# Kernel optimization log

Hardware: AMD Instinct MI355X
Metric: run time of the kernel (lower is better)

## Reference

```python
import jax, jax.numpy as jnp
import numpy as np

B, T, F, U = 32, 128, 128, 128  # batch, seq_length, feature dim, lstm units


def setup_inputs() -> dict:
    key = jax.random.key(0)
    ks = jax.random.split(key, 5)
    X = jax.random.normal(ks[0], (B, T, F), dtype=jnp.float32)
    # Dense(seq_length) over concat([X, s_repeated]) -> weight [(F+U), T]
    Wd = jax.random.normal(ks[1], (F + U, T), dtype=jnp.float32) / np.sqrt(F + U)
    bd = jnp.zeros((T,), jnp.float32)
    # Keras LSTM params, gate order i,f,c,o packed along last axis
    Wk = jax.random.normal(ks[2], (F, 4 * U), dtype=jnp.float32) / np.sqrt(F)
    Wr = jax.random.normal(ks[3], (U, 4 * U), dtype=jnp.float32) / np.sqrt(U)
    bl = jnp.zeros((4 * U,), jnp.float32)
    return {"X": X, "Wd": Wd, "bd": bd, "Wk": Wk, "Wr": Wr, "bl": bl}


def reference(X, Wd, bd, Wk, Wr, bl):
    Bq, Tq, Fq = X.shape
    Uq = Wr.shape[0]

    def step(s, i):
        # s: attention query carried across steps (= previous h_state)
        s_rep = jnp.broadcast_to(s[:, None, :], (Bq, Tq, Uq))
        concat_X = jnp.concatenate([X, s_rep], axis=-1)           # [B,T,F+U]
        alphas = jax.nn.softmax(concat_X @ Wd + bd, axis=1)        # [B,T,T], softmax over seq axis
        alpha_i = alphas[:, :, i]                                  # [B,T] (only column i is used)
        ctx = jnp.einsum('bt,btf->bf', alpha_i, X)                 # [B,F] weighted sum
        # Keras LSTM called with initial_state=None each step -> h0 = c0 = 0
        h0 = jnp.zeros((Bq, Uq), X.dtype)
        c0 = jnp.zeros((Bq, Uq), X.dtype)
        z = ctx @ Wk + h0 @ Wr + bl                                # [B,4U]
        zi, zf, zc, zo = jnp.split(z, 4, axis=-1)
        c = jax.nn.sigmoid(zf) * c0 + jax.nn.sigmoid(zi) * jnp.tanh(zc)
        h = jax.nn.sigmoid(zo) * jnp.tanh(c)                       # [B,U]
        return h, h  # new query s = h_state; per-step output = lstm_out[:, 0, :]

    s0 = jnp.zeros((Bq, Uq), X.dtype)
    _, outs = jax.lax.scan(step, s0, jnp.arange(Tq))               # [T,B,U]
    return jnp.transpose(outs, (1, 0, 2))                          # [B,T,U]
```

## Files before the change

### kernel.cpp

```cpp
#include <hip/hip_runtime.h>

namespace {

constexpr int Bq = 32;
constexpr int Tq = 128;
constexpr int Fq = 128;
constexpr int Uq = 128;
constexpr int PITCH = 129;
constexpr int APITCH = 17;

__device__ __forceinline__ float sigmoid_(float x) {
  return 1.0f / (1.0f + __expf(-x));
}
__device__ __forceinline__ float tanh_(float x) {
  x = fminf(20.0f, fmaxf(-20.0f, x));
  const float e = __expf(2.0f * x);
  return (e - 1.0f) / (e + 1.0f);
}

__global__ __launch_bounds__(256) void k_fused(const float* __restrict__ X,
                                               const float* __restrict__ Wd,
                                               float* __restrict__ C) {
  __shared__ float Xs[Tq * PITCH];
  __shared__ float As[Tq * APITCH];
  const int tid = threadIdx.x;
  const int b = blockIdx.y;
  const float* Xb = X + b * (Tq * Fq);
#pragma unroll
  for (int it = 0; it < 16; ++it) {
    const int e = tid + it * 256;
    const int t = e >> 5;
    const int f4 = e & 31;
    const float4 v = reinterpret_cast<const float4*>(Xb)[e];
    float* d = &Xs[t * PITCH + f4 * 4];
    d[0] = v.x; d[1] = v.y; d[2] = v.z; d[3] = v.w;
  }
  __syncthreads();

  const int lane = tid & 63;
  const int wv = tid >> 6;
  const int iL = wv * 4;
  const int i0 = __builtin_amdgcn_readfirstlane((int)(blockIdx.x * 16u) + iL);

  float a0[4] = {0.f, 0.f, 0.f, 0.f}, a1[4] = {0.f, 0.f, 0.f, 0.f};
  const float* Wp = Wd + i0;
  const float* xr0 = &Xs[lane * PITCH];
  const float* xr1 = &Xs[(lane + 64) * PITCH];
#pragma unroll 8
  for (int f = 0; f < Fq; ++f) {
    const float x0 = xr0[f];
    const float x1 = xr1[f];
    const float* wr = Wp + f * Tq;
#pragma unroll
    for (int j = 0; j < 4; ++j) {
      const float w = wr[j];
      a0[j] = fmaf(x0, w, a0[j]);
      a1[j] = fmaf(x1, w, a1[j]);
    }
  }

  float p0[4], p1[4];
#pragma unroll
  for (int j = 0; j < 4; ++j) {
    float m = fmaxf(a0[j], a1[j]);
#pragma unroll
    for (int d = 1; d < 64; d <<= 1) m = fmaxf(m, __shfl_xor(m, d, 64));
    const float e0 = __expf(a0[j] - m);
    const float e1 = __expf(a1[j] - m);
    float s = e0 + e1;
#pragma unroll
    for (int d = 1; d < 64; d <<= 1) s += __shfl_xor(s, d, 64);
    const float inv = 1.0f / s;
    p0[j] = e0 * inv;
    p1[j] = e1 * inv;
  }

  *reinterpret_cast<float4*>(&As[lane * APITCH + iL]) =
      make_float4(p0[0], p0[1], p0[2], p0[3]);
  *reinterpret_cast<float4*>(&As[(lane + 64) * APITCH + iL]) =
      make_float4(p1[0], p1[1], p1[2], p1[3]);
  __syncthreads();

  float c0[4] = {0.f, 0.f, 0.f, 0.f}, c1[4] = {0.f, 0.f, 0.f, 0.f};
#pragma unroll 8
  for (int t = 0; t < Tq; ++t) {
    const float4 a4 = *reinterpret_cast<const float4*>(&As[t * APITCH + iL]);
    const float aa[4] = {a4.x, a4.y, a4.z, a4.w};
    const float x0 = Xs[t * PITCH + lane];
    const float x1 = Xs[t * PITCH + lane + 64];
#pragma unroll
    for (int j = 0; j < 4; ++j) {
      c0[j] = fmaf(aa[j], x0, c0[j]);
      c1[j] = fmaf(aa[j], x1, c1[j]);
    }
  }

#pragma unroll
  for (int j = 0; j < 4; ++j) {
    float* cp = C + (b * Tq + i0 + j) * Fq;
    cp[lane] = c0[j];
    cp[lane + 64] = c1[j];
  }
}

__global__ __launch_bounds__(256) void k_out(const float* __restrict__ C,
                                             const float* __restrict__ Wk,
                                             const float* __restrict__ bl,
                                             float* __restrict__ out) {
  __shared__ float Cs[Tq * PITCH];
  const int tid = threadIdx.x;
  const int b = blockIdx.x;
  const float* Cb = C + b * (Tq * Fq);
#pragma unroll
  for (int it = 0; it < 16; ++it) {
    const int e = tid + it * 256;
    const int i = e >> 5;
    const int f4 = e & 31;
    const float4 v = reinterpret_cast<const float4*>(Cb)[e];
    float* d = &Cs[i * PITCH + f4 * 4];
    d[0] = v.x; d[1] = v.y; d[2] = v.z; d[3] = v.w;
  }
  __syncthreads();

  const int lane = tid & 63;
  const int wv = tid >> 6;
  const int u0 = __builtin_amdgcn_readfirstlane((int)(blockIdx.y * 16u) + wv * 4);

  float ai0[4] = {0.f, 0.f, 0.f, 0.f}, ai1[4] = {0.f, 0.f, 0.f, 0.f};
  float ac0[4] = {0.f, 0.f, 0.f, 0.f}, ac1[4] = {0.f, 0.f, 0.f, 0.f};
  float ao0[4] = {0.f, 0.f, 0.f, 0.f}, ao1[4] = {0.f, 0.f, 0.f, 0.f};

  const float* Wp = Wk + u0;
  const float* cr0 = &Cs[lane * PITCH];
  const float* cr1 = &Cs[(lane + 64) * PITCH];
#pragma unroll 8
  for (int f = 0; f < Fq; ++f) {
    const float c0 = cr0[f];
    const float c1 = cr1[f];
    const float* wr = Wp + f * (4 * Uq);
#pragma unroll
    for (int j = 0; j < 4; ++j) {
      const float wi = wr[j];
      const float wc = wr[2 * Uq + j];
      const float wo = wr[3 * Uq + j];
      ai0[j] = fmaf(c0, wi, ai0[j]); ai1[j] = fmaf(c1, wi, ai1[j]);
      ac0[j] = fmaf(c0, wc, ac0[j]); ac1[j] = fmaf(c1, wc, ac1[j]);
      ao0[j] = fmaf(c0, wo, ao0[j]); ao1[j] = fmaf(c1, wo, ao1[j]);
    }
  }

  float h0[4], h1[4];
#pragma unroll
  for (int j = 0; j < 4; ++j) {
    const float bi = bl[u0 + j];
    const float bc = bl[2 * Uq + u0 + j];
    const float bo = bl[3 * Uq + u0 + j];
    const float cc0 = sigmoid_(ai0[j] + bi) * tanh_(ac0[j] + bc);
    h0[j] = sigmoid_(ao0[j] + bo) * tanh_(cc0);
    const float cc1 = sigmoid_(ai1[j] + bi) * tanh_(ac1[j] + bc);
    h1[j] = sigmoid_(ao1[j] + bo) * tanh_(cc1);
  }

  float* O0 = out + ((b * Tq + lane) * Uq + u0);
  float* O1 = out + ((b * Tq + lane + 64) * Uq + u0);
  reinterpret_cast<float4*>(O0)[0] = make_float4(h0[0], h0[1], h0[2], h0[3]);
  reinterpret_cast<float4*>(O1)[0] = make_float4(h1[0], h1[1], h1[2], h1[3]);
}

}

extern "C" void kernel_launch(void* const* d_in, const int* in_sizes, int n_in,
                              void* d_out, int out_size, void* d_ws, size_t ws_size,
                              hipStream_t stream) {
  const float* X  = (const float*)d_in[0];
  const float* Wd = (const float*)d_in[1];
  const float* Wk = (const float*)d_in[3];
  const float* bl = (const float*)d_in[5];
  float* out = (float*)d_out;

  float* C = (float*)d_ws;

  k_fused<<<dim3(8, 32), 256, 0, stream>>>(X, Wd, C);
  k_out<<<dim3(32, 8), 256, 0, stream>>>(C, Wk, bl, out);
}
```

Baseline: 103.2 us.

## Fuse context and LSTM output kernels into one, keeping context tile in LDS

Merges the two kernels into one. Each block now keeps its 16-row context tile in shared memory and computes the LSTM gates and h for those rows directly, so the intermediate C buffer is never written to or read back from global memory and one launch goes away. The gate matmul is re-tiled so each thread covers one unit across 8 rows and reads float4 context values from LDS. In exchange, every block reads the Wk columns it needs from global memory (mostly L2 hits), and shared memory use per block grows slightly.

```diff
diff --git a/kernel.cpp b/kernel.cpp
--- a/kernel.cpp
+++ b/kernel.cpp
@@ -6,8 +6,10 @@
 constexpr int Tq = 128;
 constexpr int Fq = 128;
 constexpr int Uq = 128;
-constexpr int PITCH = 129;
-constexpr int APITCH = 17;
+constexpr int PITCH  = 129;
+constexpr int APITCH = 20;
+constexpr int CPITCH = 132;
+constexpr int ITILE  = 16;
 
 __device__ __forceinline__ float sigmoid_(float x) {
   return 1.0f / (1.0f + __expf(-x));
@@ -18,13 +20,18 @@
   return (e - 1.0f) / (e + 1.0f);
 }
 
-__global__ __launch_bounds__(256) void k_fused(const float* __restrict__ X,
-                                               const float* __restrict__ Wd,
-                                               float* __restrict__ C) {
+__global__ __launch_bounds__(256) void k_all(const float* __restrict__ X,
+                                             const float* __restrict__ Wd,
+                                             const float* __restrict__ Wk,
+                                             const float* __restrict__ bl,
+                                             float* __restrict__ out) {
   __shared__ float Xs[Tq * PITCH];
   __shared__ float As[Tq * APITCH];
+  __shared__ float Cs[ITILE * CPITCH];
   const int tid = threadIdx.x;
   const int b = blockIdx.y;
+  const int i0b = blockIdx.x * ITILE;
+
   const float* Xb = X + b * (Tq * Fq);
 #pragma unroll
   for (int it = 0; it < 16; ++it) {
@@ -40,7 +47,7 @@
   const int lane = tid & 63;
   const int wv = tid >> 6;
   const int iL = wv * 4;
-  const int i0 = __builtin_amdgcn_readfirstlane((int)(blockIdx.x * 16u) + iL);
+  const int i0 = __builtin_amdgcn_readfirstlane(i0b + iL);
 
   float a0[4] = {0.f, 0.f, 0.f, 0.f}, a1[4] = {0.f, 0.f, 0.f, 0.f};
   const float* Wp = Wd + i0;
@@ -94,77 +101,51 @@
       c1[j] = fmaf(aa[j], x1, c1[j]);
     }
   }
-
 #pragma unroll
   for (int j = 0; j < 4; ++j) {
-    float* cp = C + (b * Tq + i0 + j) * Fq;
-    cp[lane] = c0[j];
-    cp[lane + 64] = c1[j];
-  }
-}
-
-__global__ __launch_bounds__(256) void k_out(const float* __restrict__ C,
-                                             const float* __restrict__ Wk,
-                                             const float* __restrict__ bl,
-                                             float* __restrict__ out) {
-  __shared__ float Cs[Tq * PITCH];
-  const int tid = threadIdx.x;
-  const int b = blockIdx.x;
-  const float* Cb = C + b * (Tq * Fq);
-#pragma unroll
-  for (int it = 0; it < 16; ++it) {
-    const int e = tid + it * 256;
-    const int i = e >> 5;
-    const int f4 = e & 31;
-    const float4 v = reinterpret_cast<const float4*>(Cb)[e];
-    float* d = &Cs[i * PITCH + f4 * 4];
-    d[0] = v.x; d[1] = v.y; d[2] = v.z; d[3] = v.w;
+    Cs[(iL + j) * CPITCH + lane] = c0[j];
+    Cs[(iL + j) * CPITCH + lane + 64] = c1[j];
   }
   __syncthreads();
 
-  const int lane = tid & 63;
-  const int wv = tid >> 6;
-  const int u0 = __builtin_amdgcn_readfirstlane((int)(blockIdx.y * 16u) + wv * 4);
+  const int uu = lane & 31;
+  const int ih = (lane >> 5) * 8;
+  const int ub = wv * 32 + uu;
+  float zi[8], zc[8], zo[8];
+#pragma unroll
+  for (int j = 0; j < 8; ++j) { zi[j] = 0.f; zc[j] = 0.f; zo[j] = 0.f; }
 
-  float ai0[4] = {0.f, 0.f, 0.f, 0.f}, ai1[4] = {0.f, 0.f, 0.f, 0.f};
-  float ac0[4] = {0.f, 0.f, 0.f, 0.f}, ac1[4] = {0.f, 0.f, 0.f, 0.f};
-  float ao0[4] = {0.f, 0.f, 0.f, 0.f}, ao1[4] = {0.f, 0.f, 0.f, 0.f};
-
-  const float* Wp = Wk + u0;
-  const float* cr0 = &Cs[lane * PITCH];
-  const float* cr1 = &Cs[(lane + 64) * PITCH];
-#pragma unroll 8
-  for (int f = 0; f < Fq; ++f) {
-    const float c0 = cr0[f];
-    const float c1 = cr1[f];
-    const float* wr = Wp + f * (4 * Uq);
+  const float* WkP = Wk + ub;
+  for (int f = 0; f < Fq; f += 4) {
+    float4 cr[8];
 #pragma unroll
-    for (int j = 0; j < 4; ++j) {
-      const float wi = wr[j];
-      const float wc = wr[2 * Uq + j];
-      const float wo = wr[3 * Uq + j];
-      ai0[j] = fmaf(c0, wi, ai0[j]); ai1[j] = fmaf(c1, wi, ai1[j]);
-      ac0[j] = fmaf(c0, wc, ac0[j]); ac1[j] = fmaf(c1, wc, ac1[j]);
-      ao0[j] = fmaf(c0, wo, ao0[j]); ao1[j] = fmaf(c1, wo, ao1[j]);
+    for (int j = 0; j < 8; ++j)
+      cr[j] = *reinterpret_cast<const float4*>(&Cs[(ih + j) * CPITCH + f]);
+#pragma unroll
+    for (int ff = 0; ff < 4; ++ff) {
+      const float* wf = WkP + (f + ff) * (4 * Uq);
+      const float wi = wf[0];
+      const float wc = wf[2 * Uq];
+      const float wo = wf[3 * Uq];
+#pragma unroll
+      for (int j = 0; j < 8; ++j) {
+        const float cv = (&cr[j].x)[ff];
+        zi[j] = fmaf(cv, wi, zi[j]);
+        zc[j] = fmaf(cv, wc, zc[j]);
+        zo[j] = fmaf(cv, wo, zo[j]);
+      }
     }
   }
 
-  float h0[4], h1[4];
+  const float bi = bl[ub];
+  const float bc = bl[2 * Uq + ub];
+  const float bo = bl[3 * Uq + ub];
 #pragma unroll
-  for (int j = 0; j < 4; ++j) {
-    const float bi = bl[u0 + j];
-    const float bc = bl[2 * Uq + u0 + j];
-    const float bo = bl[3 * Uq + u0 + j];
-    const float cc0 = sigmoid_(ai0[j] + bi) * tanh_(ac0[j] + bc);
-    h0[j] = sigmoid_(ao0[j] + bo) * tanh_(cc0);
-    const float cc1 = sigmoid_(ai1[j] + bi) * tanh_(ac1[j] + bc);
-    h1[j] = sigmoid_(ao1[j] + bo) * tanh_(cc1);
+  for (int j = 0; j < 8; ++j) {
+    const float cc = sigmoid_(zi[j] + bi) * tanh_(zc[j] + bc);
+    const float h = sigmoid_(zo[j] + bo) * tanh_(cc);
+    out[(b * Tq + i0b + ih + j) * Uq + ub] = h;
   }
-
-  float* O0 = out + ((b * Tq + lane) * Uq + u0);
-  float* O1 = out + ((b * Tq + lane + 64) * Uq + u0);
-  reinterpret_cast<float4*>(O0)[0] = make_float4(h0[0], h0[1], h0[2], h0[3]);
-  reinterpret_cast<float4*>(O1)[0] = make_float4(h1[0], h1[1], h1[2], h1[3]);
 }
 
 }
@@ -178,8 +159,5 @@
   const float* bl = (const float*)d_in[5];
   float* out = (float*)d_out;
 
-  float* C = (float*)d_ws;
-
-  k_fused<<<dim3(8, 32), 256, 0, stream>>>(X, Wd, C);
-  k_out<<<dim3(32, 8), 256, 0, stream>>>(C, Wk, bl, out);
+  k_all<<<dim3(8, 32), 256, 0, stream>>>(X, Wd, Wk, bl, out);
 }
```

Result: faster. 92.17 us (-10.7%).
